# Kernel tuning notes

Hardware: AMD Instinct MI355X
Metric: run time of the kernel (lower is better)

Reference implementation:

```python
import jax, jax.numpy as jnp
import numpy as np

N_NODES = 50000
N_EDGES = 800000
IN_DIM = 128
EDGE_DIM = 32
HIDDEN = 128
NUM_LAYERS = 3
BN_EPS = 1e-5
RES_SCALE = 0.1


def setup_inputs() -> dict:
    key = jax.random.key(0)
    ks = jax.random.split(key, 10)
    x = jax.random.normal(ks[0], (N_NODES, IN_DIM), dtype=jnp.float32)
    edge_index = jax.random.randint(ks[1], (2, N_EDGES), 0, N_NODES, dtype=jnp.int64)
    edge_attr = jax.random.normal(ks[2], (N_EDGES, EDGE_DIM), dtype=jnp.float32)
    s = 0.05
    We = jax.random.normal(ks[3], (NUM_LAYERS, EDGE_DIM, HIDDEN), dtype=jnp.float32) * s
    be = jax.random.normal(ks[4], (NUM_LAYERS, HIDDEN), dtype=jnp.float32) * s
    W1 = jax.random.normal(ks[5], (NUM_LAYERS, HIDDEN, HIDDEN), dtype=jnp.float32) * s
    b1 = jax.random.normal(ks[6], (NUM_LAYERS, HIDDEN), dtype=jnp.float32) * s
    W2 = jax.random.normal(ks[7], (NUM_LAYERS, HIDDEN, HIDDEN), dtype=jnp.float32) * s
    b2 = jax.random.normal(ks[8], (NUM_LAYERS, HIDDEN), dtype=jnp.float32) * s
    gamma = jnp.ones((NUM_LAYERS, HIDDEN), dtype=jnp.float32)
    beta = jnp.zeros((NUM_LAYERS, HIDDEN), dtype=jnp.float32)
    return {"x": x, "edge_index": edge_index, "edge_attr": edge_attr,
            "We": We, "be": be, "W1": W1, "b1": b1, "W2": W2, "b2": b2,
            "gamma": gamma, "beta": beta}


def reference(x, edge_index, edge_attr, We, be, W1, b1, W2, b2, gamma, beta):
    # Dropout treated as eval-mode identity (deterministic reference).
    src = edge_index[0]  # x_j source nodes
    dst = edge_index[1]  # aggregation targets x_i
    n = x.shape[0]
    h = x
    for l in range(NUM_LAYERS):
        h_res = h
        # GINEConv message: ReLU(x_j + Linear(edge_attr)), eps=0
        e = edge_attr @ We[l] + be[l]            # [E, H]
        msg = jax.nn.relu(h[src] + e)            # [E, H]
        agg = jax.ops.segment_sum(msg, dst, num_segments=n)  # [N, H]
        z = h + agg                               # (1+eps)*x_i + sum, eps=0
        # GINE nn: Linear -> ReLU -> Linear
        z = jax.nn.relu(z @ W1[l] + b1[l]) @ W2[l] + b2[l]
        # BatchNorm over node axis (training batch stats)
        mu = jnp.mean(z, axis=0)
        var = jnp.var(z, axis=0)
        z = (z - mu) * jax.lax.rsqrt(var + BN_EPS) * gamma[l] + beta[l]
        z = jax.nn.relu(z)
        h = z + RES_SCALE * h_res
    return h
```

## Files before the change

### kernel.cpp

```cpp
#include <hip/hip_runtime.h>
#include <hip/hip_bf16.h>

#define N_NODES   50000
#define N_EDGES   800000
#define IN_DIM    128
#define EDGE_DIM  32
#define HIDDEN    128
#define NUM_LAYERS 3
#define BN_EPS    1e-5f
#define RES_SCALE 0.1f

typedef unsigned int   u32;
typedef unsigned short u16;
typedef _Float16 half2_t __attribute__((ext_vector_type(2)));
typedef _Float16 half8 __attribute__((ext_vector_type(8)));
typedef unsigned int u32x4 __attribute__((ext_vector_type(4)));
typedef float f32x4 __attribute__((ext_vector_type(4)));

#define AS4 __attribute__((address_space(4)))

__device__ __forceinline__ half2_t as_half2(u32 v) {
    union { u32 u; half2_t h; } c; c.u = v; return c.h;
}
__device__ __forceinline__ u32 pack_half2(float a, float b) {
    union { u32 u; half2_t h; } c;
    c.h.x = (_Float16)a; c.h.y = (_Float16)b; return c.u;
}

#if defined(__has_builtin)
#if __has_builtin(__builtin_amdgcn_fdot2)
#define HAVE_FDOT2 1
#endif
#endif

__device__ __forceinline__ float fdot2f(half2_t a, half2_t b, float c) {
#ifdef HAVE_FDOT2
    return __builtin_amdgcn_fdot2(a, b, c, false);
#else
    c = fmaf((float)a.x, (float)b.x, c);
    c = fmaf((float)a.y, (float)b.y, c);
    return c;
#endif
}

__global__ __launch_bounds__(256) void init_kernel(const float* __restrict__ x,
                                                   u32* __restrict__ h16,
                                                   u32* __restrict__ deg,
                                                   float* __restrict__ statsAll) {
    int idx = blockIdx.x * 256 + threadIdx.x;
    if (idx < N_NODES * 64) {
        int n = idx >> 6, l = idx & 63;
        float a = x[n * HIDDEN + l];
        float b = x[n * HIDDEN + 64 + l];
        h16[idx] = pack_half2(a, b);
    }
    if (idx < N_NODES) deg[idx] = 0u;
    if (idx < NUM_LAYERS * 256) statsAll[idx] = 0.f;
}

__global__ __launch_bounds__(256) void hist_kernel(const int* __restrict__ ei,
                                                   u32* __restrict__ deg) {
    int e = blockIdx.x * 256 + threadIdx.x;
    if (e < N_EDGES) atomicAdd(&deg[ei[N_EDGES + e]], 1u);
}

#define SCAN_NB ((N_NODES + 255) / 256)

__global__ __launch_bounds__(256) void scan1_kernel(const u32* __restrict__ deg,
                                                    u32* __restrict__ bsum) {
    int i = blockIdx.x * 256 + threadIdx.x;
    u32 v = (i < N_NODES) ? deg[i] : 0u;
    v += __shfl_down(v, 32, 64);
    v += __shfl_down(v, 16, 64);
    v += __shfl_down(v, 8, 64);
    v += __shfl_down(v, 4, 64);
    v += __shfl_down(v, 2, 64);
    v += __shfl_down(v, 1, 64);
    __shared__ u32 ws[4];
    if ((threadIdx.x & 63) == 0) ws[threadIdx.x >> 6] = v;
    __syncthreads();
    if (threadIdx.x == 0) bsum[blockIdx.x] = ws[0] + ws[1] + ws[2] + ws[3];
}

__global__ __launch_bounds__(256) void scan2_kernel(const u32* __restrict__ bsum,
                                                    u32* __restrict__ bbase,
                                                    u32* __restrict__ off) {
    __shared__ u32 tmp[256];
    int t = threadIdx.x;
    u32 v = (t < SCAN_NB) ? bsum[t] : 0u;
    tmp[t] = v;
    __syncthreads();
    for (int d = 1; d < 256; d <<= 1) {
        u32 u = (t >= d) ? tmp[t - d] : 0u;
        __syncthreads();
        tmp[t] += u;
        __syncthreads();
    }
    if (t < SCAN_NB) bbase[t] = (t == 0) ? 0u : tmp[t - 1];
    if (t == 255) off[N_NODES] = tmp[255];
}

__global__ __launch_bounds__(256) void scan3_kernel(const u32* __restrict__ deg,
                                                    const u32* __restrict__ bbase,
                                                    u32* __restrict__ off,
                                                    u32* __restrict__ cursor) {
    __shared__ u32 tmp[256];
    int t = threadIdx.x;
    int i = blockIdx.x * 256 + t;
    u32 v = (i < N_NODES) ? deg[i] : 0u;
    tmp[t] = v;
    __syncthreads();
    for (int d = 1; d < 256; d <<= 1) {
        u32 u = (t >= d) ? tmp[t - d] : 0u;
        __syncthreads();
        tmp[t] += u;
        __syncthreads();
    }
    if (i < N_NODES) {
        u32 excl = bbase[blockIdx.x] + tmp[t] - v;
        off[i] = excl;
        cursor[i] = excl;
    }
}

__global__ __launch_bounds__(256) void scatter_kernel(const int* __restrict__ ei,
                                                      u32* __restrict__ cursor,
                                                      int* __restrict__ ssrc,
                                                      const float* __restrict__ ea,
                                                      _Float16* __restrict__ ea_perm) {
    int e = blockIdx.x * 256 + threadIdx.x;
    if (e >= N_EDGES) return;
    int dst = ei[N_EDGES + e];
    u32 pos = atomicAdd(&cursor[dst], 1u);
    ssrc[pos] = ei[e];
    const float4* src = (const float4*)(ea + (size_t)e * EDGE_DIM);
    u32 buf[16];
#pragma unroll
    for (int q = 0; q < 8; q++) {
        float4 v = src[q];
        buf[2 * q + 0] = pack_half2(v.x, v.y);
        buf[2 * q + 1] = pack_half2(v.z, v.w);
    }
    uint4* dp = (uint4*)(ea_perm + (size_t)pos * EDGE_DIM);
#pragma unroll
    for (int q = 0; q < 4; q++)
        dp[q] = make_uint4(buf[4 * q], buf[4 * q + 1], buf[4 * q + 2], buf[4 * q + 3]);
}

__global__ __launch_bounds__(256) void wconv_kernel(const float* __restrict__ W1,
                                                    const float* __restrict__ W2,
                                                    _Float16* __restrict__ w1t,
                                                    _Float16* __restrict__ w2t) {
    int idx = blockIdx.x * 256 + threadIdx.x;
    if (idx >= NUM_LAYERS * 128 * 128) return;
    int kk = idx & 127, f = (idx >> 7) & 127, l = idx >> 14;
    int k1 = (kk & 1) ? 64 + (kk >> 1) : (kk >> 1);
    w1t[idx] = (_Float16)W1[l * 16384 + k1 * 128 + f];
    w2t[idx] = (_Float16)W2[l * 16384 + kk * 128 + f];
}

__device__ __forceinline__ void edot4(const u32x4* __restrict__ d,
                                      const half2_t* __restrict__ wlo,
                                      const half2_t* __restrict__ whi,
                                      float& dl, float& dh) {
#pragma unroll
    for (int q = 0; q < 4; q++) {
        u32x4 v = d[q];
        dl = fdot2f(as_half2(v.x), wlo[q * 4 + 0], dl);
        dh = fdot2f(as_half2(v.x), whi[q * 4 + 0], dh);
        dl = fdot2f(as_half2(v.y), wlo[q * 4 + 1], dl);
        dh = fdot2f(as_half2(v.y), whi[q * 4 + 1], dh);
        dl = fdot2f(as_half2(v.z), wlo[q * 4 + 2], dl);
        dh = fdot2f(as_half2(v.z), whi[q * 4 + 2], dh);
        dl = fdot2f(as_half2(v.w), wlo[q * 4 + 3], dl);
        dh = fdot2f(as_half2(v.w), whi[q * 4 + 3], dh);
    }
}

__global__ __launch_bounds__(256) void agg_perm_kernel(
    const u32* __restrict__ h16, const _Float16* __restrict__ ea_perm,
    const int* __restrict__ ssrc, const u32* __restrict__ off,
    const float* __restrict__ We, const float* __restrict__ be,
    u32* __restrict__ z16) {
    int t = threadIdx.x;
    int lane = t & 63;
    half2_t wlo[16], whi[16];
#pragma unroll
    for (int k = 0; k < 16; k++) {
        half2_t a, b;
        a.x = (_Float16)We[(2 * k + 0) * HIDDEN + lane];
        a.y = (_Float16)We[(2 * k + 1) * HIDDEN + lane];
        b.x = (_Float16)We[(2 * k + 0) * HIDDEN + 64 + lane];
        b.y = (_Float16)We[(2 * k + 1) * HIDDEN + 64 + lane];
        wlo[k] = a; whi[k] = b;
    }
    float blo = be[lane], bhi = be[64 + lane];

    const AS4 int*   cssrc = (const AS4 int*)(unsigned long long)ssrc;
    const AS4 u32*   coff  = (const AS4 u32*)(unsigned long long)off;
    const AS4 u32x4* cea   = (const AS4 u32x4*)(unsigned long long)ea_perm;

    int wid = __builtin_amdgcn_readfirstlane(t >> 6);
    int slot = blockIdx.x * 4 + wid;
    int nslots = gridDim.x * 4;
    for (int n = slot; n < N_NODES; n += nslots) {
        int e0 = (int)coff[n], e1 = (int)coff[n + 1];
        float al0 = 0.f, ah0 = 0.f, al1 = 0.f, ah1 = 0.f;
        int e = e0;
        if (e + 2 <= e1) {
            int s0 = cssrc[e], s1 = cssrc[e + 1];
            u32x4 A0[4], A1[4];
#pragma unroll
            for (int q = 0; q < 4; q++) { A0[q] = cea[e * 4 + q]; A1[q] = cea[e * 4 + 4 + q]; }
            while (true) {
                u32 g0 = h16[s0 * 64 + lane];
                u32 g1 = h16[s1 * 64 + lane];
                int en = e + 2;
                int more = (en + 2 <= e1);
                float d0l = 0.f, d0h = 0.f, d1l = 0.f, d1h = 0.f;
                edot4(A0, wlo, whi, d0l, d0h);
                edot4(A1, wlo, whi, d1l, d1h);
                int ns0 = s0, ns1 = s1;
                if (more) {
                    ns0 = cssrc[en]; ns1 = cssrc[en + 1];
#pragma unroll
                    for (int q = 0; q < 4; q++) { A0[q] = cea[en * 4 + q]; A1[q] = cea[en * 4 + 4 + q]; }
                }
                half2_t hh0 = as_half2(g0), hh1 = as_half2(g1);
                al0 += fmaxf(d0l + blo + (float)hh0.x, 0.f);
                ah0 += fmaxf(d0h + bhi + (float)hh0.y, 0.f);
                al1 += fmaxf(d1l + blo + (float)hh1.x, 0.f);
                ah1 += fmaxf(d1h + bhi + (float)hh1.y, 0.f);
                e = en;
                if (!more) break;
                s0 = ns0; s1 = ns1;
            }
        }
        if (e < e1) {
            int s0 = cssrc[e];
            u32x4 A0[4];
#pragma unroll
            for (int q = 0; q < 4; q++) A0[q] = cea[e * 4 + q];
            float dl = 0.f, dh = 0.f;
            edot4(A0, wlo, whi, dl, dh);
            half2_t hh = as_half2(h16[s0 * 64 + lane]);
            al0 += fmaxf(dl + blo + (float)hh.x, 0.f);
            ah0 += fmaxf(dh + bhi + (float)hh.y, 0.f);
        }
        half2_t self = as_half2(h16[n * 64 + lane]);
        z16[n * 64 + lane] = pack_half2((float)self.x + al0 + al1,
                                        (float)self.y + ah0 + ah1);
    }
}

__global__ __launch_bounds__(256) void mlp_mfma_kernel(
    const u32* __restrict__ z16,
    const _Float16* __restrict__ w1t, const float* __restrict__ b1_,
    const _Float16* __restrict__ w2t, const float* __restrict__ b2_,
    float* __restrict__ z2, float* __restrict__ stats) {
    __shared__ __align__(16) char lds[65536];
    char* zh = lds;
    char* wh = lds + 32768;
    int t = threadIdx.x, l = t & 63, w = t >> 6;
    int li = l & 15, rg = l >> 4;
    int base = blockIdx.x * 128;

#pragma unroll
    for (int rep = 0; rep < 8; rep++) {
        int c = t + rep * 256;
        int n = c >> 4, s = c & 15;
        int gn = base + n;
        uint4 v = make_uint4(0u, 0u, 0u, 0u);
        if (gn < N_NODES) v = *(const uint4*)(z16 + (size_t)gn * 64 + s * 4);
        *(uint4*)(zh + n * 256 + ((s ^ (n & 7)) << 4)) = v;
    }
#pragma unroll
    for (int rep = 0; rep < 8; rep++) {
        int c = t + rep * 256;
        int f = c >> 4, s = c & 15;
        uint4 v = *(const uint4*)((const char*)w1t + f * 256 + s * 16);
        *(uint4*)(wh + f * 256 + ((s ^ (f & 7)) << 4)) = v;
    }
    __syncthreads();

    int f0 = w * 32 + li;
    int f1 = w * 32 + 16 + li;

    f32x4 acc0[8], acc1[8];
    {
        float bva = b1_[f0], bvb = b1_[f1];
#pragma unroll
        for (int m = 0; m < 8; m++) {
            acc0[m] = (f32x4){bva, bva, bva, bva};
            acc1[m] = (f32x4){bvb, bvb, bvb, bvb};
        }
    }
#pragma unroll
    for (int kt = 0; kt < 4; kt++) {
        int s = kt * 4 + rg;
        half8 bf0 = *(const half8*)(wh + f0 * 256 + ((s ^ (f0 & 7)) << 4));
        half8 bf1 = *(const half8*)(wh + f1 * 256 + ((s ^ (f1 & 7)) << 4));
#pragma unroll
        for (int m = 0; m < 8; m++) {
            int n = m * 16 + li;
            half8 af = *(const half8*)(zh + n * 256 + ((s ^ (n & 7)) << 4));
            acc0[m] = __builtin_amdgcn_mfma_f32_16x16x32_f16(af, bf0, acc0[m], 0, 0, 0);
            acc1[m] = __builtin_amdgcn_mfma_f32_16x16x32_f16(af, bf1, acc1[m], 0, 0, 0);
        }
    }
    __syncthreads();

#pragma unroll
    for (int m = 0; m < 8; m++) {
#pragma unroll
        for (int r = 0; r < 4; r++) {
            int n = m * 16 + rg * 4 + r;
            int s0 = f0 >> 3;
            *(_Float16*)(zh + n * 256 + ((s0 ^ (n & 7)) << 4) + (f0 & 7) * 2) =
                (_Float16)fmaxf(acc0[m][r], 0.f);
            int s1 = f1 >> 3;
            *(_Float16*)(zh + n * 256 + ((s1 ^ (n & 7)) << 4) + (f1 & 7) * 2) =
                (_Float16)fmaxf(acc1[m][r], 0.f);
        }
    }
#pragma unroll
    for (int rep = 0; rep < 8; rep++) {
        int c = t + rep * 256;
        int f = c >> 4, s = c & 15;
        uint4 v = *(const uint4*)((const char*)w2t + f * 256 + s * 16);
        *(uint4*)(wh + f * 256 + ((s ^ (f & 7)) << 4)) = v;
    }
    __syncthreads();

    {
        float cva = b2_[f0], cvb = b2_[f1];
#pragma unroll
        for (int m = 0; m < 8; m++) {
            acc0[m] = (f32x4){cva, cva, cva, cva};
            acc1[m] = (f32x4){cvb, cvb, cvb, cvb};
        }
    }
#pragma unroll
    for (int kt = 0; kt < 4; kt++) {
        int s = kt * 4 + rg;
        half8 bf0 = *(const half8*)(wh + f0 * 256 + ((s ^ (f0 & 7)) << 4));
        half8 bf1 = *(const half8*)(wh + f1 * 256 + ((s ^ (f1 & 7)) << 4));
#pragma unroll
        for (int m = 0; m < 8; m++) {
            int n = m * 16 + li;
            half8 af = *(const half8*)(zh + n * 256 + ((s ^ (n & 7)) << 4));
            acc0[m] = __builtin_amdgcn_mfma_f32_16x16x32_f16(af, bf0, acc0[m], 0, 0, 0);
            acc1[m] = __builtin_amdgcn_mfma_f32_16x16x32_f16(af, bf1, acc1[m], 0, 0, 0);
        }
    }

    float s0 = 0.f, q0 = 0.f, s1 = 0.f, q1 = 0.f;
#pragma unroll
    for (int m = 0; m < 8; m++) {
#pragma unroll
        for (int r = 0; r < 4; r++) {
            int gn = base + m * 16 + rg * 4 + r;
            if (gn < N_NODES) {
                float v0 = acc0[m][r], v1 = acc1[m][r];
                z2[(size_t)gn * 128 + f0] = v0;
                z2[(size_t)gn * 128 + f1] = v1;
                s0 += v0; q0 = fmaf(v0, v0, q0);
                s1 += v1; q1 = fmaf(v1, v1, q1);
            }
        }
    }
    s0 += __shfl_xor(s0, 16); s0 += __shfl_xor(s0, 32);
    q0 += __shfl_xor(q0, 16); q0 += __shfl_xor(q0, 32);
    s1 += __shfl_xor(s1, 16); s1 += __shfl_xor(s1, 32);
    q1 += __shfl_xor(q1, 16); q1 += __shfl_xor(q1, 32);
    if (rg == 0) {
        unsafeAtomicAdd(&stats[f0], s0);
        unsafeAtomicAdd(&stats[128 + f0], q0);
        unsafeAtomicAdd(&stats[f1], s1);
        unsafeAtomicAdd(&stats[128 + f1], q1);
    }
}

__global__ __launch_bounds__(256) void bn_kernel(
    const float* __restrict__ z2, const float* __restrict__ stats,
    const float* __restrict__ gamma, const float* __restrict__ beta,
    u32* __restrict__ h16, float* __restrict__ out, int write_out) {
    int idx = blockIdx.x * 256 + threadIdx.x;
    if (idx >= N_NODES * 64) return;
    int n = idx >> 6, l = idx & 63;
    const float inv_n = 1.0f / (float)N_NODES;
    float mu_l = stats[l] * inv_n;
    float mu_h = stats[64 + l] * inv_n;
    float var_l = stats[HIDDEN + l] * inv_n - mu_l * mu_l;
    float var_h = stats[HIDDEN + 64 + l] * inv_n - mu_h * mu_h;
    float inv_l = rsqrtf(var_l + BN_EPS);
    float inv_h = rsqrtf(var_h + BN_EPS);
    float zl = (z2[n * HIDDEN + l]      - mu_l) * inv_l * gamma[l]      + beta[l];
    float zh = (z2[n * HIDDEN + 64 + l] - mu_h) * inv_h * gamma[64 + l] + beta[64 + l];
    zl = fmaxf(zl, 0.f);
    zh = fmaxf(zh, 0.f);
    half2_t hh = as_half2(h16[idx]);
    float hn_l = fmaf(RES_SCALE, (float)hh.x, zl);
    float hn_h = fmaf(RES_SCALE, (float)hh.y, zh);
    h16[idx] = pack_half2(hn_l, hn_h);
    if (write_out) {
        out[n * HIDDEN + l] = hn_l;
        out[n * HIDDEN + 64 + l] = hn_h;
    }
}

extern "C" void kernel_launch(void* const* d_in, const int* in_sizes, int n_in,
                              void* d_out, int out_size, void* d_ws, size_t ws_size,
                              hipStream_t stream) {
    const float* x     = (const float*)d_in[0];
    const int*   ei    = (const int*)d_in[1];
    const float* ea    = (const float*)d_in[2];
    const float* We    = (const float*)d_in[3];
    const float* be    = (const float*)d_in[4];
    const float* W1    = (const float*)d_in[5];
    const float* b1    = (const float*)d_in[6];
    const float* W2    = (const float*)d_in[7];
    const float* b2    = (const float*)d_in[8];
    const float* gamma = (const float*)d_in[9];
    const float* beta  = (const float*)d_in[10];
    float* out = (float*)d_out;

    char* wsp = (char*)d_ws;
    const size_t NH = (size_t)N_NODES * HIDDEN;
    u32*      h16    = (u32*)wsp;      wsp += (size_t)N_NODES * 64 * 4;
    u32*      z16    = (u32*)wsp;      wsp += (size_t)N_NODES * 64 * 4;
    float*    z2     = (float*)wsp;    wsp += NH * 4;
    _Float16* ea_perm= (_Float16*)wsp; wsp += (size_t)N_EDGES * EDGE_DIM * 2;
    _Float16* w1t    = (_Float16*)wsp; wsp += (size_t)NUM_LAYERS * 128 * 128 * 2;
    _Float16* w2t    = (_Float16*)wsp; wsp += (size_t)NUM_LAYERS * 128 * 128 * 2;
    float*    statsA = (float*)wsp;    wsp += (size_t)NUM_LAYERS * 256 * 4;
    u32*      deg    = (u32*)wsp;      wsp += (size_t)N_NODES * 4;
    u32*      cursor = (u32*)wsp;      wsp += (size_t)N_NODES * 4;
    int*      ssrc   = (int*)wsp;      wsp += (size_t)N_EDGES * 4;
    u32*      off    = (u32*)wsp;      wsp += (size_t)(N_NODES + 1) * 4;
    u32*      bsum   = (u32*)wsp;      wsp += (size_t)SCAN_NB * 4;
    u32*      bbase  = (u32*)wsp;      wsp += (size_t)SCAN_NB * 4;

    const int p_blocks  = (N_NODES * 64 + 255) / 256;
    const int e_blocks  = (N_EDGES + 255) / 256;
    const int m_blocks  = (N_NODES + 127) / 128;
    const int w_blocks  = (NUM_LAYERS * 128 * 128 + 255) / 256;

    init_kernel<<<p_blocks, 256, 0, stream>>>(x, h16, deg, statsA);
    hist_kernel<<<e_blocks, 256, 0, stream>>>(ei, deg);
    scan1_kernel<<<SCAN_NB, 256, 0, stream>>>(deg, bsum);
    scan2_kernel<<<1, 256, 0, stream>>>(bsum, bbase, off);
    scan3_kernel<<<SCAN_NB, 256, 0, stream>>>(deg, bbase, off, cursor);
    scatter_kernel<<<e_blocks, 256, 0, stream>>>(ei, cursor, ssrc, ea, ea_perm);
    wconv_kernel<<<w_blocks, 256, 0, stream>>>(W1, W2, w1t, w2t);

    for (int l = 0; l < NUM_LAYERS; l++) {
        agg_perm_kernel<<<4096, 256, 0, stream>>>(
            h16, ea_perm, ssrc, off,
            We + (size_t)l * EDGE_DIM * HIDDEN, be + (size_t)l * HIDDEN, z16);
        mlp_mfma_kernel<<<m_blocks, 256, 0, stream>>>(
            z16, w1t + (size_t)l * 16384, b1 + (size_t)l * HIDDEN,
            w2t + (size_t)l * 16384, b2 + (size_t)l * HIDDEN,
            z2, statsA + (size_t)l * 256);
        bn_kernel<<<p_blocks, 256, 0, stream>>>(
            z2, statsA + (size_t)l * 256, gamma + (size_t)l * HIDDEN, beta + (size_t)l * HIDDEN,
            h16, out, (l == NUM_LAYERS - 1) ? 1 : 0);
    }
}
```

Measured before the change: 623.4 us.

## Compute edge-linear messages with MFMA in aggregation and permute hidden-feature layout

Replaces the per-lane fdot2 edge projection in the aggregation kernel with 16x16x32 f16 MFMA over tiles of 16 incoming edges, with a pre-transposed We fragment buffer. The hidden-state storage is permuted so that each lane gathers a uint4 of source features matching the MFMA output layout, and the init, BN and W1 conversion kernels are adjusted to that layout. This aims to cut the ALU cost of the per-edge 32x128 projection. In exchange, partial tiles waste MFMA work (nodes average 16 edges) and the tail path reads ssrc and edge attributes past the segment end, then masks them.

```diff
diff --git a/kernel.cpp b/kernel.cpp
--- a/kernel.cpp
+++ b/kernel.cpp
@@ -27,32 +27,16 @@
     c.h.x = (_Float16)a; c.h.y = (_Float16)b; return c.u;
 }
 
-#if defined(__has_builtin)
-#if __has_builtin(__builtin_amdgcn_fdot2)
-#define HAVE_FDOT2 1
-#endif
-#endif
-
-__device__ __forceinline__ float fdot2f(half2_t a, half2_t b, float c) {
-#ifdef HAVE_FDOT2
-    return __builtin_amdgcn_fdot2(a, b, c, false);
-#else
-    c = fmaf((float)a.x, (float)b.x, c);
-    c = fmaf((float)a.y, (float)b.y, c);
-    return c;
-#endif
-}
-
 __global__ __launch_bounds__(256) void init_kernel(const float* __restrict__ x,
                                                    u32* __restrict__ h16,
                                                    u32* __restrict__ deg,
                                                    float* __restrict__ statsAll) {
     int idx = blockIdx.x * 256 + threadIdx.x;
     if (idx < N_NODES * 64) {
-        int n = idx >> 6, l = idx & 63;
-        float a = x[n * HIDDEN + l];
-        float b = x[n * HIDDEN + 64 + l];
-        h16[idx] = pack_half2(a, b);
+        int n = idx >> 6, w = idx & 63;
+        int li = w >> 2, q = w & 3;
+        int f = q * 16 + li;
+        h16[idx] = pack_half2(x[n * HIDDEN + f], x[n * HIDDEN + 64 + f]);
     }
     if (idx < N_NODES) deg[idx] = 0u;
     if (idx < NUM_LAYERS * 256) statsAll[idx] = 0.f;
@@ -149,107 +133,137 @@
 
 __global__ __launch_bounds__(256) void wconv_kernel(const float* __restrict__ W1,
                                                     const float* __restrict__ W2,
+                                                    const float* __restrict__ We,
                                                     _Float16* __restrict__ w1t,
-                                                    _Float16* __restrict__ w2t) {
+                                                    _Float16* __restrict__ w2t,
+                                                    _Float16* __restrict__ weT) {
     int idx = blockIdx.x * 256 + threadIdx.x;
-    if (idx >= NUM_LAYERS * 128 * 128) return;
-    int kk = idx & 127, f = (idx >> 7) & 127, l = idx >> 14;
-    int k1 = (kk & 1) ? 64 + (kk >> 1) : (kk >> 1);
-    w1t[idx] = (_Float16)W1[l * 16384 + k1 * 128 + f];
-    w2t[idx] = (_Float16)W2[l * 16384 + kk * 128 + f];
-}
-
-__device__ __forceinline__ void edot4(const u32x4* __restrict__ d,
-                                      const half2_t* __restrict__ wlo,
-                                      const half2_t* __restrict__ whi,
-                                      float& dl, float& dh) {
-#pragma unroll
-    for (int q = 0; q < 4; q++) {
-        u32x4 v = d[q];
-        dl = fdot2f(as_half2(v.x), wlo[q * 4 + 0], dl);
-        dh = fdot2f(as_half2(v.x), whi[q * 4 + 0], dh);
-        dl = fdot2f(as_half2(v.y), wlo[q * 4 + 1], dl);
-        dh = fdot2f(as_half2(v.y), whi[q * 4 + 1], dh);
-        dl = fdot2f(as_half2(v.z), wlo[q * 4 + 2], dl);
-        dh = fdot2f(as_half2(v.z), whi[q * 4 + 2], dh);
-        dl = fdot2f(as_half2(v.w), wlo[q * 4 + 3], dl);
-        dh = fdot2f(as_half2(v.w), whi[q * 4 + 3], dh);
-    }
-}
-
-__global__ __launch_bounds__(256) void agg_perm_kernel(
-    const u32* __restrict__ h16, const _Float16* __restrict__ ea_perm,
+    if (idx < NUM_LAYERS * 128 * 128) {
+        int kk = idx & 127, f = (idx >> 7) & 127, l = idx >> 14;
+        int w = kk >> 1;
+        int k1 = 32 * (w >> 4) + (w & 15) + ((kk & 1) << 4);
+        w1t[idx] = (_Float16)W1[l * 16384 + k1 * 128 + f];
+        w2t[idx] = (_Float16)W2[l * 16384 + kk * 128 + f];
+    }
+    if (idx < NUM_LAYERS * 8 * 64) {
+        int lane = idx & 63, c = (idx >> 6) & 7, l = idx >> 9;
+        int rg = lane >> 4, li = lane & 15;
+        _Float16* dst = weT + (size_t)idx * 8;
+#pragma unroll
+        for (int j = 0; j < 8; j++)
+            dst[j] = (_Float16)We[l * (EDGE_DIM * HIDDEN) + (8 * rg + j) * HIDDEN + c * 16 + li];
+    }
+}
+
+__global__ __launch_bounds__(256) void agg_mfma_kernel(
+    const u32* __restrict__ h16p, const _Float16* __restrict__ ea_perm,
     const int* __restrict__ ssrc, const u32* __restrict__ off,
-    const float* __restrict__ We, const float* __restrict__ be,
-    u32* __restrict__ z16) {
-    int t = threadIdx.x;
-    int lane = t & 63;
-    half2_t wlo[16], whi[16];
-#pragma unroll
-    for (int k = 0; k < 16; k++) {
-        half2_t a, b;
-        a.x = (_Float16)We[(2 * k + 0) * HIDDEN + lane];
-        a.y = (_Float16)We[(2 * k + 1) * HIDDEN + lane];
-        b.x = (_Float16)We[(2 * k + 0) * HIDDEN + 64 + lane];
-        b.y = (_Float16)We[(2 * k + 1) * HIDDEN + 64 + lane];
-        wlo[k] = a; whi[k] = b;
-    }
-    float blo = be[lane], bhi = be[64 + lane];
-
-    const AS4 int*   cssrc = (const AS4 int*)(unsigned long long)ssrc;
-    const AS4 u32*   coff  = (const AS4 u32*)(unsigned long long)off;
-    const AS4 u32x4* cea   = (const AS4 u32x4*)(unsigned long long)ea_perm;
+    const _Float16* __restrict__ weT, const float* __restrict__ be,
+    u32* __restrict__ z16b) {
+    int t = threadIdx.x, l = t & 63, li = l & 15, rg = l >> 4;
+
+    half8 bfrag[8];
+    const uint4* wp = (const uint4*)weT;
+#pragma unroll
+    for (int c = 0; c < 8; c++) {
+        union { uint4 u; half8 h; } cv;
+        cv.u = wp[c * 64 + l];
+        bfrag[c] = cv.h;
+    }
+    float beC[8];
+#pragma unroll
+    for (int c = 0; c < 8; c++) beC[c] = be[c * 16 + li];
+
+    const AS4 u32* coff = (const AS4 u32*)(unsigned long long)off;
 
     int wid = __builtin_amdgcn_readfirstlane(t >> 6);
     int slot = blockIdx.x * 4 + wid;
     int nslots = gridDim.x * 4;
     for (int n = slot; n < N_NODES; n += nslots) {
         int e0 = (int)coff[n], e1 = (int)coff[n + 1];
-        float al0 = 0.f, ah0 = 0.f, al1 = 0.f, ah1 = 0.f;
-        int e = e0;
-        if (e + 2 <= e1) {
-            int s0 = cssrc[e], s1 = cssrc[e + 1];
-            u32x4 A0[4], A1[4];
-#pragma unroll
-            for (int q = 0; q < 4; q++) { A0[q] = cea[e * 4 + q]; A1[q] = cea[e * 4 + 4 + q]; }
-            while (true) {
-                u32 g0 = h16[s0 * 64 + lane];
-                u32 g1 = h16[s1 * 64 + lane];
-                int en = e + 2;
-                int more = (en + 2 <= e1);
-                float d0l = 0.f, d0h = 0.f, d1l = 0.f, d1h = 0.f;
-                edot4(A0, wlo, whi, d0l, d0h);
-                edot4(A1, wlo, whi, d1l, d1h);
-                int ns0 = s0, ns1 = s1;
-                if (more) {
-                    ns0 = cssrc[en]; ns1 = cssrc[en + 1];
-#pragma unroll
-                    for (int q = 0; q < 4; q++) { A0[q] = cea[en * 4 + q]; A1[q] = cea[en * 4 + 4 + q]; }
+        f32x4 acc[8];
+#pragma unroll
+        for (int c = 0; c < 8; c++) acc[c] = (f32x4){0.f, 0.f, 0.f, 0.f};
+
+        for (int et = e0; et < e1; et += 16) {
+            union { uint4 u; half8 h; } av;
+            av.u = *(const uint4*)(ea_perm + (size_t)(et + li) * 32 + rg * 8);
+            f32x4 d[8];
+#pragma unroll
+            for (int c = 0; c < 8; c++) {
+                f32x4 ci = (f32x4){beC[c], beC[c], beC[c], beC[c]};
+                d[c] = __builtin_amdgcn_mfma_f32_16x16x32_f16(av.h, bfrag[c], ci, 0, 0, 0);
+            }
+            int eb = et + 4 * rg;
+            if (et + 16 <= e1) {
+                int s0 = ssrc[eb], s1 = ssrc[eb + 1], s2 = ssrc[eb + 2], s3 = ssrc[eb + 3];
+                uint4 g0 = *(const uint4*)(h16p + (size_t)s0 * 64 + li * 4);
+                uint4 g1 = *(const uint4*)(h16p + (size_t)s1 * 64 + li * 4);
+                uint4 g2 = *(const uint4*)(h16p + (size_t)s2 * 64 + li * 4);
+                uint4 g3 = *(const uint4*)(h16p + (size_t)s3 * 64 + li * 4);
+                const uint4 g[4] = {g0, g1, g2, g3};
+#pragma unroll
+                for (int r = 0; r < 4; r++) {
+                    u32 w0 = (&g[r].x)[0], w1 = (&g[r].x)[1];
+                    u32 w2 = (&g[r].x)[2], w3 = (&g[r].x)[3];
+                    acc[0][r] += fmaxf(d[0][r] + (float)as_half2(w0).x, 0.f);
+                    acc[4][r] += fmaxf(d[4][r] + (float)as_half2(w0).y, 0.f);
+                    acc[1][r] += fmaxf(d[1][r] + (float)as_half2(w1).x, 0.f);
+                    acc[5][r] += fmaxf(d[5][r] + (float)as_half2(w1).y, 0.f);
+                    acc[2][r] += fmaxf(d[2][r] + (float)as_half2(w2).x, 0.f);
+                    acc[6][r] += fmaxf(d[6][r] + (float)as_half2(w2).y, 0.f);
+                    acc[3][r] += fmaxf(d[3][r] + (float)as_half2(w3).x, 0.f);
+                    acc[7][r] += fmaxf(d[7][r] + (float)as_half2(w3).y, 0.f);
                 }
-                half2_t hh0 = as_half2(g0), hh1 = as_half2(g1);
-                al0 += fmaxf(d0l + blo + (float)hh0.x, 0.f);
-                ah0 += fmaxf(d0h + bhi + (float)hh0.y, 0.f);
-                al1 += fmaxf(d1l + blo + (float)hh1.x, 0.f);
-                ah1 += fmaxf(d1h + bhi + (float)hh1.y, 0.f);
-                e = en;
-                if (!more) break;
-                s0 = ns0; s1 = ns1;
+            } else {
+                int sv[4];
+                bool vd[4];
+#pragma unroll
+                for (int r = 0; r < 4; r++) {
+                    int ee = eb + r;
+                    int s = ssrc[ee];
+                    vd[r] = (ee < e1);
+                    sv[r] = vd[r] ? s : 0;
+                }
+#pragma unroll
+                for (int r = 0; r < 4; r++) {
+                    uint4 g = *(const uint4*)(h16p + (size_t)sv[r] * 64 + li * 4);
+                    u32 w0 = g.x, w1 = g.y, w2 = g.z, w3 = g.w;
+                    float m0 = fmaxf(d[0][r] + (float)as_half2(w0).x, 0.f);
+                    float m4 = fmaxf(d[4][r] + (float)as_half2(w0).y, 0.f);
+                    float m1 = fmaxf(d[1][r] + (float)as_half2(w1).x, 0.f);
+                    float m5 = fmaxf(d[5][r] + (float)as_half2(w1).y, 0.f);
+                    float m2 = fmaxf(d[2][r] + (float)as_half2(w2).x, 0.f);
+                    float m6 = fmaxf(d[6][r] + (float)as_half2(w2).y, 0.f);
+                    float m3 = fmaxf(d[3][r] + (float)as_half2(w3).x, 0.f);
+                    float m7 = fmaxf(d[7][r] + (float)as_half2(w3).y, 0.f);
+                    if (vd[r]) {
+                        acc[0][r] += m0; acc[1][r] += m1; acc[2][r] += m2; acc[3][r] += m3;
+                        acc[4][r] += m4; acc[5][r] += m5; acc[6][r] += m6; acc[7][r] += m7;
+                    }
+                }
             }
         }
-        if (e < e1) {
-            int s0 = cssrc[e];
-            u32x4 A0[4];
-#pragma unroll
-            for (int q = 0; q < 4; q++) A0[q] = cea[e * 4 + q];
-            float dl = 0.f, dh = 0.f;
-            edot4(A0, wlo, whi, dl, dh);
-            half2_t hh = as_half2(h16[s0 * 64 + lane]);
-            al0 += fmaxf(dl + blo + (float)hh.x, 0.f);
-            ah0 += fmaxf(dh + bhi + (float)hh.y, 0.f);
-        }
-        half2_t self = as_half2(h16[n * 64 + lane]);
-        z16[n * 64 + lane] = pack_half2((float)self.x + al0 + al1,
-                                        (float)self.y + ah0 + ah1);
+
+        float s[8];
+#pragma unroll
+        for (int c = 0; c < 8; c++) {
+            float v = acc[c][0] + acc[c][1] + acc[c][2] + acc[c][3];
+            v += __shfl_xor(v, 16);
+            v += __shfl_xor(v, 32);
+            s[c] = v;
+        }
+        float x0 = (rg & 1) ? s[2] : s[0];
+        float x1 = (rg & 1) ? s[6] : s[4];
+        float va = (rg & 2) ? x1 : x0;
+        float y0 = (rg & 1) ? s[3] : s[1];
+        float y1 = (rg & 1) ? s[7] : s[5];
+        float vb = (rg & 2) ? y1 : y0;
+        const u32* hp = h16p + (size_t)n * 64 + li * 4 + 2 * (rg & 1);
+        u32 ga = hp[0], gb = hp[1];
+        float hva = (rg >= 2) ? (float)as_half2(ga).y : (float)as_half2(ga).x;
+        float hvb = (rg >= 2) ? (float)as_half2(gb).y : (float)as_half2(gb).x;
+        z16b[(size_t)n * 64 + l] = pack_half2(hva + va, hvb + vb);
     }
 }
 
@@ -387,16 +401,18 @@
     u32* __restrict__ h16, float* __restrict__ out, int write_out) {
     int idx = blockIdx.x * 256 + threadIdx.x;
     if (idx >= N_NODES * 64) return;
-    int n = idx >> 6, l = idx & 63;
+    int n = idx >> 6, w = idx & 63;
+    int li = w >> 2, q = w & 3;
+    int f = q * 16 + li, fh = f + 64;
     const float inv_n = 1.0f / (float)N_NODES;
-    float mu_l = stats[l] * inv_n;
-    float mu_h = stats[64 + l] * inv_n;
-    float var_l = stats[HIDDEN + l] * inv_n - mu_l * mu_l;
-    float var_h = stats[HIDDEN + 64 + l] * inv_n - mu_h * mu_h;
+    float mu_l = stats[f] * inv_n;
+    float mu_h = stats[fh] * inv_n;
+    float var_l = stats[HIDDEN + f] * inv_n - mu_l * mu_l;
+    float var_h = stats[HIDDEN + fh] * inv_n - mu_h * mu_h;
     float inv_l = rsqrtf(var_l + BN_EPS);
     float inv_h = rsqrtf(var_h + BN_EPS);
-    float zl = (z2[n * HIDDEN + l]      - mu_l) * inv_l * gamma[l]      + beta[l];
-    float zh = (z2[n * HIDDEN + 64 + l] - mu_h) * inv_h * gamma[64 + l] + beta[64 + l];
+    float zl = (z2[n * HIDDEN + f]  - mu_l) * inv_l * gamma[f]  + beta[f];
+    float zh = (z2[n * HIDDEN + fh] - mu_h) * inv_h * gamma[fh] + beta[fh];
     zl = fmaxf(zl, 0.f);
     zh = fmaxf(zh, 0.f);
     half2_t hh = as_half2(h16[idx]);
@@ -404,8 +420,8 @@
     float hn_h = fmaf(RES_SCALE, (float)hh.y, zh);
     h16[idx] = pack_half2(hn_l, hn_h);
     if (write_out) {
-        out[n * HIDDEN + l] = hn_l;
-        out[n * HIDDEN + 64 + l] = hn_h;
+        out[n * HIDDEN + f]  = hn_l;
+        out[n * HIDDEN + fh] = hn_h;
     }
 }
 
@@ -433,6 +449,7 @@
     _Float16* ea_perm= (_Float16*)wsp; wsp += (size_t)N_EDGES * EDGE_DIM * 2;
     _Float16* w1t    = (_Float16*)wsp; wsp += (size_t)NUM_LAYERS * 128 * 128 * 2;
     _Float16* w2t    = (_Float16*)wsp; wsp += (size_t)NUM_LAYERS * 128 * 128 * 2;
+    _Float16* weT    = (_Float16*)wsp; wsp += (size_t)NUM_LAYERS * 4096 * 2;
     float*    statsA = (float*)wsp;    wsp += (size_t)NUM_LAYERS * 256 * 4;
     u32*      deg    = (u32*)wsp;      wsp += (size_t)N_NODES * 4;
     u32*      cursor = (u32*)wsp;      wsp += (size_t)N_NODES * 4;
@@ -452,12 +469,12 @@
     scan2_kernel<<<1, 256, 0, stream>>>(bsum, bbase, off);
     scan3_kernel<<<SCAN_NB, 256, 0, stream>>>(deg, bbase, off, cursor);
     scatter_kernel<<<e_blocks, 256, 0, stream>>>(ei, cursor, ssrc, ea, ea_perm);
-    wconv_kernel<<<w_blocks, 256, 0, stream>>>(W1, W2, w1t, w2t);
+    wconv_kernel<<<w_blocks, 256, 0, stream>>>(W1, W2, We, w1t, w2t, weT);
 
     for (int l = 0; l < NUM_LAYERS; l++) {
-        agg_perm_kernel<<<4096, 256, 0, stream>>>(
+        agg_mfma_kernel<<<4096, 256, 0, stream>>>(
             h16, ea_perm, ssrc, off,
-            We + (size_t)l * EDGE_DIM * HIDDEN, be + (size_t)l * HIDDEN, z16);
+            weT + (size_t)l * 4096, be + (size_t)l * HIDDEN, z16);
         mlp_mfma_kernel<<<m_blocks, 256, 0, stream>>>(
             z16, w1t + (size_t)l * 16384, b1 + (size_t)l * HIDDEN,
             w2t + (size_t)l * 16384, b2 + (size_t)l * HIDDEN,
```

Result: slower. 679.0 us (+8.9%).
